# Optimization experiments

Measured on AMD Instinct MI355X. Metric: run time of the kernel, lower is better.

The kernel has to match this reference:

```python
import jax, jax.numpy as jnp
import numpy as np

OUT, IN = 4096, 4096
B, S = 2, 2048

def setup_inputs() -> dict:
    key = jax.random.key(0)
    k1, k2, k3, k4 = jax.random.split(key, 4)
    x = jax.random.normal(k1, (B, S, IN), dtype=jnp.float32)
    # symmetric int8 quantized weight [out, in]
    weight_q = jax.random.randint(k2, (OUT, IN), -128, 128, dtype=jnp.int32).astype(jnp.int8)
    # per-output-channel scale, small positive (like |w|_max/127)
    scale = (jax.random.uniform(k3, (1, OUT), dtype=jnp.float32) * 0.01 + 1e-4)
    bias = jax.random.normal(k4, (OUT,), dtype=jnp.float32)
    return {"x": x, "weight_q": weight_q, "scale": scale, "bias": bias}

def reference(x, weight_q, scale, bias):
    # out = (x_2d @ W_q^T (dequantized)) * scale + bias
    x2d = x.reshape(-1, x.shape[-1])                       # [B*S, in]
    w = weight_q.astype(x.dtype)                            # dequant cast [out, in]
    out = jnp.einsum('ni,oi->no', x2d, w) * scale           # [B*S, out] * [1, out]
    out = out.reshape(x.shape[:-1] + (out.shape[-1],))
    return out + bias
```

## Files before the change

kernel.cpp:

```cpp
#include <hip/hip_runtime.h>
#include <stdint.h>


#define M_DIM 4096
#define N_DIM 4096
#define K_DIM 4096
#define BM 256
#define BN 256
#define BK 32
#define KT_N (K_DIM / BK)
#define TILE_SHORTS 8192

typedef _Float16 f16x8 __attribute__((ext_vector_type(8)));
typedef __bf16   bf16x8v __attribute__((ext_vector_type(8)));
typedef float    f32x4 __attribute__((ext_vector_type(4)));

__device__ __forceinline__ unsigned short f32_f16_bits(float f) {
    _Float16 h = (_Float16)f;
    return __builtin_bit_cast(unsigned short, h);
}

__device__ __forceinline__ void gld16(const unsigned short* g, unsigned short* l) {
    __builtin_amdgcn_global_load_lds(
        (const __attribute__((address_space(1))) unsigned int*)g,
        (__attribute__((address_space(3))) unsigned int*)l,
        16, 0, 0);
}

__global__ __launch_bounds__(256) void cvt_x_f16(const float* __restrict__ x,
                                                 unsigned short* __restrict__ AT) {
    const int b  = blockIdx.x;
    const int mi = b >> 7;
    const int kt = b & 127;
    const int r  = threadIdx.x;

    const float* xp = x + (size_t)(mi * 256 + r) * K_DIM + kt * 32;
    unsigned short hh[32];
    #pragma unroll
    for (int j4 = 0; j4 < 8; ++j4) {
        float4 v = *(const float4*)(xp + j4 * 4);
        hh[j4*4+0] = f32_f16_bits(v.x);
        hh[j4*4+1] = f32_f16_bits(v.y);
        hh[j4*4+2] = f32_f16_bits(v.z);
        hh[j4*4+3] = f32_f16_bits(v.w);
    }
    unsigned short* o = AT + (size_t)(mi * KT_N + kt) * TILE_SHORTS + r * 8;
    #pragma unroll
    for (int ks = 0; ks < 4; ++ks) {
        uint4 p;
        p.x = (unsigned)hh[ks*8+0] | ((unsigned)hh[ks*8+1] << 16);
        p.y = (unsigned)hh[ks*8+2] | ((unsigned)hh[ks*8+3] << 16);
        p.z = (unsigned)hh[ks*8+4] | ((unsigned)hh[ks*8+5] << 16);
        p.w = (unsigned)hh[ks*8+6] | ((unsigned)hh[ks*8+7] << 16);
        *(uint4*)(o + ks * 2048) = p;
    }
}

__global__ __launch_bounds__(256) void cvt_w_f16(const int* __restrict__ wq,
                                                 unsigned short* __restrict__ BT) {
    const int b  = blockIdx.x;
    const int ni = b >> 7;
    const int kt = b & 127;
    const int c  = threadIdx.x;

    const int* wp = wq + (size_t)(ni * 256 + c) * K_DIM + kt * 32;
    unsigned short bb[32];
    #pragma unroll
    for (int j4 = 0; j4 < 8; ++j4) {
        int4 v = *(const int4*)(wp + j4 * 4);
        bb[j4*4+0] = f32_f16_bits((float)v.x);
        bb[j4*4+1] = f32_f16_bits((float)v.y);
        bb[j4*4+2] = f32_f16_bits((float)v.z);
        bb[j4*4+3] = f32_f16_bits((float)v.w);
    }
    unsigned short* ob = BT + (size_t)(ni * KT_N + kt) * TILE_SHORTS + c * 8;
    #pragma unroll
    for (int ks = 0; ks < 4; ++ks) {
        uint4 p;
        p.x = (unsigned)bb[ks*8+0] | ((unsigned)bb[ks*8+1] << 16);
        p.y = (unsigned)bb[ks*8+2] | ((unsigned)bb[ks*8+3] << 16);
        p.z = (unsigned)bb[ks*8+4] | ((unsigned)bb[ks*8+5] << 16);
        p.w = (unsigned)bb[ks*8+6] | ((unsigned)bb[ks*8+7] << 16);
        *(uint4*)(ob + ks * 2048) = p;
    }
}

__global__ __launch_bounds__(512, 2) void gemm_pipe(
    const unsigned short* __restrict__ AT,
    const unsigned short* __restrict__ BT,
    const float* __restrict__ scale, const float* __restrict__ bias,
    float* __restrict__ out)
{
    __shared__ unsigned short lds[3 * TILE_SHORTS];

    const int t    = threadIdx.x;
    const int lane = t & 63;
    const int wid  = t >> 6;
    const int wr   = wid >> 2;
    const int wc   = wid & 3;
    const int lr   = lane & 15;
    const int ksf  = lane >> 4;

    const int bid = blockIdx.x;
    const int swz = (bid & 7) * 32 + (bid >> 3);
    const int mi  = swz & 15;
    const int ni  = swz >> 4;

    const int lb0 = (t & ~63) * 8;
    const int lb1 = lb0 + 4096;
    const unsigned short* gA = AT + (size_t)mi * KT_N * TILE_SHORTS + t * 8;

#define STAGE_A(bufbase, kt) do { \
    gld16(gA + (size_t)(kt) * TILE_SHORTS,        lds + (bufbase) + lb0); \
    gld16(gA + (size_t)(kt) * TILE_SHORTS + 4096, lds + (bufbase) + lb1); \
} while (0)

    const unsigned short* gBf = BT + (size_t)ni * KT_N * TILE_SHORTS
                               + (ksf * 256 + wc * 64 + lr) * 8;

    const int baseA = (ksf * 256 + wr * 128 + lr) * 8;

    f32x4 acc[8][4];
    #pragma unroll
    for (int m = 0; m < 8; ++m)
        #pragma unroll
        for (int n = 0; n < 4; ++n)
            acc[m][n] = (f32x4){0.f, 0.f, 0.f, 0.f};

    f16x8 bE[4], bO[4];

#define KSTEP(kt, rB, sB, bCUR, bNXT) do {                                    \
    const unsigned short* Lb = lds + (rB);                                    \
    f16x8 aF[8];                                                              \
    _Pragma("unroll")                                                         \
    for (int m = 0; m < 8; ++m) aF[m] = *(const f16x8*)(Lb + baseA + m*128);  \
    if ((kt) + 1 < KT_N) {                                                    \
        const unsigned short* gb = gBf + (size_t)((kt) + 1) * TILE_SHORTS;    \
        _Pragma("unroll")                                                     \
        for (int n = 0; n < 4; ++n) bNXT[n] = *(const f16x8*)(gb + n * 128);  \
    }                                                                         \
    if ((kt) + 2 < KT_N) STAGE_A((sB), (kt) + 2);                             \
    __builtin_amdgcn_s_setprio(1);                                            \
    _Pragma("unroll")                                                         \
    for (int m = 0; m < 8; ++m)                                               \
        _Pragma("unroll")                                                     \
        for (int n = 0; n < 4; ++n)                                           \
            acc[m][n] = __builtin_amdgcn_mfma_f32_16x16x32_f16(               \
                aF[m], bCUR[n], acc[m][n], 0, 0, 0);                          \
    __builtin_amdgcn_s_setprio(0);                                            \
    if ((kt) + 2 < KT_N) asm volatile("s_waitcnt vmcnt(2) lgkmcnt(0)" ::: "memory"); \
    else                 asm volatile("s_waitcnt vmcnt(0) lgkmcnt(0)" ::: "memory"); \
    __builtin_amdgcn_s_barrier();                                             \
} while (0)

    STAGE_A(0, 0);
    STAGE_A(TILE_SHORTS, 1);
    #pragma unroll
    for (int n = 0; n < 4; ++n) bE[n] = *(const f16x8*)(gBf + n * 128);
    asm volatile("s_waitcnt vmcnt(0)" ::: "memory");
    __builtin_amdgcn_s_barrier();

    int rB = 0;
    int sB = 2 * TILE_SHORTS;
    for (int kt2 = 0; kt2 < KT_N; kt2 += 2) {
        KSTEP(kt2,     rB, sB, bE, bO);
        rB = (rB == 2*TILE_SHORTS) ? 0 : rB + TILE_SHORTS;
        sB = (sB == 2*TILE_SHORTS) ? 0 : sB + TILE_SHORTS;
        KSTEP(kt2 + 1, rB, sB, bO, bE);
        rB = (rB == 2*TILE_SHORTS) ? 0 : rB + TILE_SHORTS;
        sB = (sB == 2*TILE_SHORTS) ? 0 : sB + TILE_SHORTS;
    }
#undef KSTEP
#undef STAGE_A

    #pragma unroll
    for (int n = 0; n < 4; ++n) {
        const int col = ni * BN + wc * 64 + n * 16 + lr;
        const float sc = scale[col];
        const float bi = bias[col];
        #pragma unroll
        for (int m = 0; m < 8; ++m) {
            const int r0 = mi * BM + wr * 128 + m * 16 + ksf * 4;
            #pragma unroll
            for (int j = 0; j < 4; ++j)
                out[(size_t)(r0 + j) * N_DIM + col] = acc[m][n][j] * sc + bi;
        }
    }
}

__device__ __forceinline__ unsigned short f32_bf16_rne(float f) {
    unsigned u = __float_as_uint(f);
    u += 0x7FFFu + ((u >> 16) & 1u);
    return (unsigned short)(u >> 16);
}

__device__ __forceinline__ void cvt2(float a, float b, unsigned& hi2, unsigned& lo2) {
    unsigned short ha = f32_bf16_rne(a), hb = f32_bf16_rne(b);
    float fa = __uint_as_float((unsigned)ha << 16);
    float fb = __uint_as_float((unsigned)hb << 16);
    unsigned short la = f32_bf16_rne(a - fa), lb = f32_bf16_rne(b - fb);
    hi2 = (unsigned)ha | ((unsigned)hb << 16);
    lo2 = (unsigned)la | ((unsigned)lb << 16);
}

__global__ __launch_bounds__(256) void gemm_fb(
    const float* __restrict__ X, const int* __restrict__ Wq,
    const float* __restrict__ scale, const float* __restrict__ bias,
    float* __restrict__ out)
{
    __shared__ unsigned short sAh[4 * 128 * 8];
    __shared__ unsigned short sAl[4 * 128 * 8];
    __shared__ unsigned short sB [4 * 128 * 8];

    const int t    = threadIdx.x;
    const int lane = t & 63;
    const int wid  = t >> 6;
    const int brow = blockIdx.y * 128;
    const int bcol = blockIdx.x * 128;

    const int c1 = t,        c2 = t + 256;
    const int r1 = c1 & 127, s1 = c1 >> 7;
    const int r2 = c2 & 127, s2 = c2 >> 7;

    const int wr  = wid >> 1, wc = wid & 1;
    const int lr  = lane & 15;
    const int ksf = lane >> 4;

    f32x4 acc[4][4];
    #pragma unroll
    for (int m = 0; m < 4; ++m)
        #pragma unroll
        for (int n = 0; n < 4; ++n)
            acc[m][n] = (f32x4){0.f, 0.f, 0.f, 0.f};

    for (int k0 = 0; k0 < K_DIM; k0 += 32) {
        #pragma unroll
        for (int cc = 0; cc < 2; ++cc) {
            const int c = cc ? c2 : c1;
            const int r = cc ? r2 : r1;
            const int s = cc ? s2 : s1;
            const float* xa = X + (size_t)(brow + r) * K_DIM + k0 + s * 8;
            float4 v0 = *(const float4*)(xa);
            float4 v1 = *(const float4*)(xa + 4);
            uint4 hv, lv;
            cvt2(v0.x, v0.y, hv.x, lv.x);
            cvt2(v0.z, v0.w, hv.y, lv.y);
            cvt2(v1.x, v1.y, hv.z, lv.z);
            cvt2(v1.z, v1.w, hv.w, lv.w);
            *(uint4*)(sAh + c * 8) = hv;
            *(uint4*)(sAl + c * 8) = lv;

            const int* wa = Wq + (size_t)(bcol + r) * K_DIM + k0 + s * 8;
            int4 w0 = *(const int4*)(wa);
            int4 w1 = *(const int4*)(wa + 4);
            uint4 wv;
            wv.x = (unsigned)f32_bf16_rne((float)w0.x) | ((unsigned)f32_bf16_rne((float)w0.y) << 16);
            wv.y = (unsigned)f32_bf16_rne((float)w0.z) | ((unsigned)f32_bf16_rne((float)w0.w) << 16);
            wv.z = (unsigned)f32_bf16_rne((float)w1.x) | ((unsigned)f32_bf16_rne((float)w1.y) << 16);
            wv.w = (unsigned)f32_bf16_rne((float)w1.z) | ((unsigned)f32_bf16_rne((float)w1.w) << 16);
            *(uint4*)(sB + c * 8) = wv;
        }
        __syncthreads();

        bf16x8v ah[4], al[4], bb[4];
        #pragma unroll
        for (int m = 0; m < 4; ++m) {
            const int row = wr * 64 + m * 16 + lr;
            ah[m] = *(const bf16x8v*)(sAh + (ksf * 128 + row) * 8);
            al[m] = *(const bf16x8v*)(sAl + (ksf * 128 + row) * 8);
        }
        #pragma unroll
        for (int n = 0; n < 4; ++n) {
            const int row = wc * 64 + n * 16 + lr;
            bb[n] = *(const bf16x8v*)(sB + (ksf * 128 + row) * 8);
        }

        #pragma unroll
        for (int m = 0; m < 4; ++m)
            #pragma unroll
            for (int n = 0; n < 4; ++n) {
                acc[m][n] = __builtin_amdgcn_mfma_f32_16x16x32_bf16(ah[m], bb[n], acc[m][n], 0, 0, 0);
                acc[m][n] = __builtin_amdgcn_mfma_f32_16x16x32_bf16(al[m], bb[n], acc[m][n], 0, 0, 0);
            }
        __syncthreads();
    }

    #pragma unroll
    for (int n = 0; n < 4; ++n) {
        const int col = bcol + wc * 64 + n * 16 + lr;
        const float sc = scale[col];
        const float bi = bias[col];
        #pragma unroll
        for (int m = 0; m < 4; ++m) {
            const int r0 = brow + wr * 64 + m * 16 + ksf * 4;
            #pragma unroll
            for (int j = 0; j < 4; ++j)
                out[(size_t)(r0 + j) * N_DIM + col] = acc[m][n][j] * sc + bi;
        }
    }
}

extern "C" void kernel_launch(void* const* d_in, const int* in_sizes, int n_in,
                              void* d_out, int out_size, void* d_ws, size_t ws_size,
                              hipStream_t stream) {
    const float* x     = (const float*)d_in[0];
    const int*   wq    = (const int*)d_in[1];
    const float* scale = (const float*)d_in[2];
    const float* bias  = (const float*)d_in[3];
    float*       out   = (float*)d_out;

    const size_t planeElems = (size_t)M_DIM * K_DIM;
    const size_t planeBytes = planeElems * sizeof(unsigned short);

    if (ws_size >= 2 * planeBytes) {
        unsigned short* AT = (unsigned short*)d_ws;
        unsigned short* BT = AT + planeElems;
        cvt_x_f16<<<2048, 256, 0, stream>>>(x, AT);
        cvt_w_f16<<<2048, 256, 0, stream>>>(wq, BT);
        gemm_pipe<<<(M_DIM / BM) * (N_DIM / BN), 512, 0, stream>>>(AT, BT, scale, bias, out);
    } else {
        dim3 grid(N_DIM / 128, M_DIM / 128);
        gemm_fb<<<grid, 256, 0, stream>>>(x, wq, scale, bias, out);
    }
}
```

Measured before the change: 168.0 us.

## Software-pipeline GEMM k-loop so MFMAs use previous step's fragments

Restructures the main k-loop so each step issues LDS reads of the current A fragments and the A staging for step s+2, then runs the MFMAs on the previous step's A and B fragments, then loads the next B from global. The aim is to hide LDS and global load latency behind the MFMA block, with the final MFMA batch peeled after the loop. It adds a second set of A fragment registers, which raises VGPR pressure. It also relaxes the vmcnt waits, and their correctness depends on the exact count of outstanding loads.

```diff
diff --git a/kernel.cpp b/kernel.cpp
--- a/kernel.cpp
+++ b/kernel.cpp
@@ -127,29 +127,31 @@
         for (int n = 0; n < 4; ++n)
             acc[m][n] = (f32x4){0.f, 0.f, 0.f, 0.f};
 
-    f16x8 bE[4], bO[4];
-
-#define KSTEP(kt, rB, sB, bCUR, bNXT) do {                                    \
+    f16x8 aE[8], aO[8], bE[4], bO[4];
+
+#define KSTEP(s, rB, sB, aCUR, aPRV, bX) do {                                 \
     const unsigned short* Lb = lds + (rB);                                    \
-    f16x8 aF[8];                                                              \
     _Pragma("unroll")                                                         \
-    for (int m = 0; m < 8; ++m) aF[m] = *(const f16x8*)(Lb + baseA + m*128);  \
-    if ((kt) + 1 < KT_N) {                                                    \
-        const unsigned short* gb = gBf + (size_t)((kt) + 1) * TILE_SHORTS;    \
+    for (int m = 0; m < 8; ++m) aCUR[m] = *(const f16x8*)(Lb + baseA + m*128);\
+    if ((s) + 2 < KT_N) STAGE_A((sB), (s) + 2);                               \
+    if ((s) > 0) {                                                            \
+        __builtin_amdgcn_s_setprio(1);                                        \
         _Pragma("unroll")                                                     \
-        for (int n = 0; n < 4; ++n) bNXT[n] = *(const f16x8*)(gb + n * 128);  \
+        for (int m = 0; m < 8; ++m)                                           \
+            _Pragma("unroll")                                                 \
+            for (int n = 0; n < 4; ++n)                                       \
+                acc[m][n] = __builtin_amdgcn_mfma_f32_16x16x32_f16(           \
+                    aPRV[m], bX[n], acc[m][n], 0, 0, 0);                      \
+        __builtin_amdgcn_s_setprio(0);                                        \
     }                                                                         \
-    if ((kt) + 2 < KT_N) STAGE_A((sB), (kt) + 2);                             \
-    __builtin_amdgcn_s_setprio(1);                                            \
-    _Pragma("unroll")                                                         \
-    for (int m = 0; m < 8; ++m)                                               \
+    if ((s) + 1 < KT_N) {                                                     \
+        const unsigned short* gb = gBf + (size_t)((s) + 1) * TILE_SHORTS;     \
         _Pragma("unroll")                                                     \
-        for (int n = 0; n < 4; ++n)                                           \
-            acc[m][n] = __builtin_amdgcn_mfma_f32_16x16x32_f16(               \
-                aF[m], bCUR[n], acc[m][n], 0, 0, 0);                          \
-    __builtin_amdgcn_s_setprio(0);                                            \
-    if ((kt) + 2 < KT_N) asm volatile("s_waitcnt vmcnt(2) lgkmcnt(0)" ::: "memory"); \
-    else                 asm volatile("s_waitcnt vmcnt(0) lgkmcnt(0)" ::: "memory"); \
+        for (int n = 0; n < 4; ++n) bX[n] = *(const f16x8*)(gb + n * 128);    \
+    }                                                                         \
+    if ((s) + 2 < KT_N)      asm volatile("s_waitcnt vmcnt(6) lgkmcnt(0)" ::: "memory"); \
+    else if ((s) + 1 < KT_N) asm volatile("s_waitcnt vmcnt(4) lgkmcnt(0)" ::: "memory"); \
+    else                     asm volatile("s_waitcnt vmcnt(0) lgkmcnt(0)" ::: "memory"); \
     __builtin_amdgcn_s_barrier();                                             \
 } while (0)
 
@@ -157,19 +159,26 @@
     STAGE_A(TILE_SHORTS, 1);
     #pragma unroll
     for (int n = 0; n < 4; ++n) bE[n] = *(const f16x8*)(gBf + n * 128);
-    asm volatile("s_waitcnt vmcnt(0)" ::: "memory");
+    asm volatile("s_waitcnt vmcnt(6)" ::: "memory");
     __builtin_amdgcn_s_barrier();
 
     int rB = 0;
     int sB = 2 * TILE_SHORTS;
-    for (int kt2 = 0; kt2 < KT_N; kt2 += 2) {
-        KSTEP(kt2,     rB, sB, bE, bO);
+    for (int s2 = 0; s2 < KT_N; s2 += 2) {
+        KSTEP(s2,     rB, sB, aE, aO, bO);
         rB = (rB == 2*TILE_SHORTS) ? 0 : rB + TILE_SHORTS;
         sB = (sB == 2*TILE_SHORTS) ? 0 : sB + TILE_SHORTS;
-        KSTEP(kt2 + 1, rB, sB, bO, bE);
+        KSTEP(s2 + 1, rB, sB, aO, aE, bE);
         rB = (rB == 2*TILE_SHORTS) ? 0 : rB + TILE_SHORTS;
         sB = (sB == 2*TILE_SHORTS) ? 0 : sB + TILE_SHORTS;
     }
+    __builtin_amdgcn_s_setprio(1);
+    #pragma unroll
+    for (int m = 0; m < 8; ++m)
+        #pragma unroll
+        for (int n = 0; n < 4; ++n)
+            acc[m][n] = __builtin_amdgcn_mfma_f32_16x16x32_f16(aO[m], bO[n], acc[m][n], 0, 0, 0);
+    __builtin_amdgcn_s_setprio(0);
 #undef KSTEP
 #undef STAGE_A
 
```

Measured after the change: 165.5 us. About the same (-1.5%).
